# Kernel optimization log

Measured on AMD Instinct MI355X. Metric: run time of the kernel, lower is better.

The kernel has to match this reference:

```python
import jax, jax.numpy as jnp
import numpy as np

B, N = 64, 512
D_ENT, H = 2000, 768
LN_EPS = 1e-12


def setup_inputs() -> dict:
    key = jax.random.key(0)
    ks = jax.random.split(key, 16)
    s = 1.0 / np.sqrt(D_ENT)
    sh = 1.0 / np.sqrt(H)
    return {
        "node_embeddings": jax.random.normal(ks[0], (B, N, D_ENT), jnp.float32),
        "node_types": jax.random.randint(ks[1], (B, N), 0, 2),
        "layers": jax.random.randint(ks[2], (B, N), 0, 8),
        "operators": jax.random.randint(ks[3], (B, N), 0, 2),
        "in_degs": jax.random.randint(ks[4], (B, N), 0, 8),
        "out_degs": jax.random.randint(ks[5], (B, N), 0, 8),
        "negs": jax.random.randint(ks[6], (B, N), 0, 2),
        "type_emb": jax.random.normal(ks[7], (2, H), jnp.float32),
        "layer_emb": jax.random.normal(ks[8], (8, H), jnp.float32),
        "op_emb": jax.random.normal(ks[9], (2, H), jnp.float32),
        "in_emb": jax.random.normal(ks[10], (8, H), jnp.float32),
        "out_emb": jax.random.normal(ks[11], (8, H), jnp.float32),
        "proj_w": jax.random.uniform(ks[12], (H, D_ENT), jnp.float32, -s, s),
        "proj_b": jnp.zeros((H,), jnp.float32),
        "neg_w": jax.random.uniform(ks[13], (H, H), jnp.float32, -sh, sh),
        "neg_b": jnp.zeros((H,), jnp.float32),
        "ln_g": jnp.ones((H,), jnp.float32),
        "ln_b": jnp.zeros((H,), jnp.float32),
    }


def reference(node_embeddings, node_types, layers, operators, in_degs, out_degs, negs,
              type_emb, layer_emb, op_emb, in_emb, out_emb,
              proj_w, proj_b, neg_w, neg_b, ln_g, ln_b):
    # linear projection: [B,N,D_ENT] @ [D_ENT,H]
    x = jnp.einsum("bnd,hd->bnh", node_embeddings, proj_w) + proj_b
    # summed small-table lookups
    x = x + type_emb[node_types] + layer_emb[layers] + op_emb[operators] \
        + in_emb[in_degs] + out_emb[out_degs]
    # rows with negs==1 go through MLP (single Linear h->h); masked select/scatter
    y = jnp.einsum("bnh,gh->bng", x, neg_w) + neg_b
    x = jnp.where((negs == 1)[..., None], y, x)
    # LayerNorm
    mu = jnp.mean(x, axis=-1, keepdims=True)
    var = jnp.mean(jnp.square(x - mu), axis=-1, keepdims=True)
    x = (x - mu) * jax.lax.rsqrt(var + LN_EPS) * ln_g + ln_b
    # dropout is identity in eval mode
    return x
```

## Files before the change

### kernel.cpp

```cpp
#include <hip/hip_runtime.h>
#include <stdint.h>

typedef unsigned short u16;
typedef short v8s __attribute__((ext_vector_type(8)));
typedef float v4f __attribute__((ext_vector_type(4)));

typedef __attribute__((address_space(1))) uint32_t g_u32;
typedef __attribute__((address_space(3))) uint32_t l_u32;

__device__ __forceinline__ void glds16(const void* g, void* l) {
    __builtin_amdgcn_global_load_lds((const g_u32*)g, (l_u32*)l, 16, 0, 0);
}
__device__ __forceinline__ u16 f2b(float f) {
    uint32_t u = __builtin_bit_cast(uint32_t, f);
    u += 0x7FFFu + ((u >> 16) & 1u);
    return (u16)(u >> 16);
}
__device__ __forceinline__ uint32_t pk2(float a, float b) {
    uint32_t ua = __builtin_bit_cast(uint32_t, a) + 0x8000u;
    uint32_t ub = __builtin_bit_cast(uint32_t, b) + 0x8000u;
    return __builtin_amdgcn_perm(ub, ua, 0x07060302u);
}

#define MTOT  32768
#define HDIM  768
#define KDIM  2000
#define KPAD  2016

#define VMW(n) asm volatile("s_waitcnt vmcnt(" #n ")" ::: "memory")
#define BARX do { __builtin_amdgcn_s_barrier(); __builtin_amdgcn_sched_barrier(0); } while (0)

__global__ __launch_bounds__(256) void cvt_weights(
    const float* __restrict__ pw, const float* __restrict__ nw,
    u16* __restrict__ Wb, u16* __restrict__ NWb)
{
    const int h = blockIdx.x;
    const float* src = pw + (size_t)h * KDIM;
    u16* dst = Wb + (size_t)h * KPAD;
    for (int k = threadIdx.x; k < KPAD; k += 256)
        dst[k] = (k < KDIM) ? f2b(src[k]) : (u16)0;
    const float* s2 = nw + (size_t)h * HDIM;
    u16* d2 = NWb + (size_t)h * HDIM;
    for (int k = threadIdx.x; k < HDIM; k += 256)
        d2[k] = f2b(s2[k]);
}

__global__ __launch_bounds__(256) void compact_k(
    const int* __restrict__ negs, int* __restrict__ cmap,
    int* __restrict__ pos, int* __restrict__ cnt)
{
    __shared__ int pref[257];
    const int t = threadIdx.x;
    const int base = t * 128;
    int c = 0;
    for (int j = 0; j < 128; j++) c += (negs[base + j] == 1);
    __shared__ int wsum[256];
    wsum[t] = c;
    __syncthreads();
    if (t == 0) {
        int a = 0;
        for (int i = 0; i < 256; i++) { pref[i] = a; a += wsum[i]; }
        pref[256] = a;
        cnt[0] = a;
    }
    __syncthreads();
    int off = pref[t];
    for (int j = 0; j < 128; j++) {
        const int r = base + j;
        if (negs[r] == 1) { cmap[off] = r; pos[r] = off; off++; }
    }
    const int total = pref[256];
    for (int j = total + t; j < MTOT; j += 256) cmap[j] = 0;
}

__global__ __launch_bounds__(512, 4) void gemm1(
    const float* __restrict__ A, const u16* __restrict__ Wb,
    const float* __restrict__ pb,
    const int* __restrict__ i_ty, const int* __restrict__ i_la,
    const int* __restrict__ i_op, const int* __restrict__ i_in, const int* __restrict__ i_ou,
    const float* __restrict__ te, const float* __restrict__ le, const float* __restrict__ oe,
    const float* __restrict__ ie, const float* __restrict__ ooe,
    u16* __restrict__ Xb)
{
    __shared__ __align__(16) float Asf[2][128 * 32];
    __shared__ __align__(16) u16  Bs[2][256 * 32];

    const int bid = blockIdx.x;
    const int sw = (bid & 7) * 96 + (bid >> 3);
    const int mt = sw / 3, nt = sw % 3;
    const int m_base = mt * 128, n_base = nt * 256;

    const int tid = threadIdx.x;
    const int w = tid >> 6, lane = tid & 63;
    const int lm = lane & 15, quad = lane >> 4;
    const int wm = (w >> 2) * 64, wn = (w & 3) * 64;

    const float* aRowBase[2];
    int aOff[2], aBase[2];
#pragma unroll
    for (int t = 0; t < 2; t++) {
        const int rl = w * 16 + t * 8 + (lane >> 3);
        aRowBase[t] = A + (size_t)(m_base + rl) * KDIM;
        aOff[t] = ((lane & 7) ^ (rl & 7)) * 4;
        aBase[t] = (w * 16 + t * 8) * 32;
    }
    const u16* bSrc[2];
    int bBase[2];
#pragma unroll
    for (int t = 0; t < 2; t++) {
        const int rl = w * 32 + t * 16 + (lane >> 2);
        const int c = (lane & 3) ^ ((rl >> 1) & 3);
        bSrc[t] = Wb + (size_t)(n_base + rl) * KPAD + c * 8;
        bBase[t] = (w * 32 + t * 16) * 32;
    }

    v4f acc[4][4];
#pragma unroll
    for (int i = 0; i < 4; i++)
#pragma unroll
        for (int j = 0; j < 4; j++) acc[i][j] = (v4f){0.f, 0.f, 0.f, 0.f};

    auto issue = [&](int kb) {
        const int sl = kb & 1;
#pragma unroll
        for (int t = 0; t < 2; t++) {
            int k = kb * 32 + aOff[t];
            k = (k > 1996) ? 1996 : k;
            glds16(aRowBase[t] + k, &Asf[sl][aBase[t]]);
        }
#pragma unroll
        for (int t = 0; t < 2; t++)
            glds16(bSrc[t] + kb * 32, &Bs[sl][bBase[t]]);
    };
    auto compute = [&](int kb) {
        const int sl = kb & 1;
        v8s af[4], bf[4];
#pragma unroll
        for (int i = 0; i < 4; i++) {
            const int r = wm + i * 16 + lm;
            const int s8 = r & 7;
            const float4 lo = *(const float4*)&Asf[sl][r * 32 + (((2 * quad)     ^ s8) << 2)];
            const float4 hi = *(const float4*)&Asf[sl][r * 32 + (((2 * quad + 1) ^ s8) << 2)];
            int4 p;
            p.x = (int)pk2(lo.x, lo.y); p.y = (int)pk2(lo.z, lo.w);
            p.z = (int)pk2(hi.x, hi.y); p.w = (int)pk2(hi.z, hi.w);
            af[i] = __builtin_bit_cast(v8s, p);
        }
#pragma unroll
        for (int j = 0; j < 4; j++) {
            const int r = wn + j * 16 + lm;
            bf[j] = *(const v8s*)&Bs[sl][r * 32 + ((quad ^ ((r >> 1) & 3)) << 3)];
        }
#pragma unroll
        for (int i = 0; i < 4; i++)
#pragma unroll
            for (int j = 0; j < 4; j++)
                acc[i][j] = __builtin_amdgcn_mfma_f32_16x16x32_bf16(af[i], bf[j], acc[i][j], 0, 0, 0);
    };

    issue(0);
    issue(1);

    for (int kb = 0; kb < 61; ++kb) {
        VMW(4);
        BARX;
        compute(kb);
        __builtin_amdgcn_sched_barrier(0);
        BARX;
        issue(kb + 2);
    }
    VMW(4); BARX; compute(61);
    __builtin_amdgcn_sched_barrier(0);
    BARX;
    VMW(0); BARX; compute(62);

#pragma unroll
    for (int i = 0; i < 4; i++) {
#pragma unroll
        for (int r = 0; r < 4; r++) {
            const int row = m_base + wm + i * 16 + quad * 4 + r;
            const int ty = i_ty[row], la = i_la[row], op = i_op[row];
            const int di = i_in[row], doo = i_ou[row];
            const float* pte = te + (size_t)ty * HDIM;
            const float* ple = le + (size_t)la * HDIM;
            const float* poe = oe + (size_t)op * HDIM;
            const float* pie = ie + (size_t)di * HDIM;
            const float* pou = ooe + (size_t)doo * HDIM;
            u16* orow = Xb + (size_t)row * HDIM;
#pragma unroll
            for (int j = 0; j < 4; j++) {
                const int col = n_base + wn + j * 16 + lm;
                float v = acc[i][j][r] + pb[col] + pte[col] + ple[col] + poe[col] + pie[col] + pou[col];
                orow[col] = f2b(v);
            }
        }
    }
}

__global__ __launch_bounds__(512, 4) void gemm2(
    const u16* __restrict__ Xb, const u16* __restrict__ NWb,
    const float* __restrict__ nb, const int* __restrict__ cmap,
    const int* __restrict__ cnt, u16* __restrict__ Yb)
{
    __shared__ __align__(16) u16 As[2][128 * 32];
    __shared__ __align__(16) u16 Bs[2][256 * 32];

    const int bid = blockIdx.x;
    const int sw = (bid & 7) * 96 + (bid >> 3);
    const int mt = sw / 3, nt = sw % 3;
    const int m_base = mt * 128, n_base = nt * 256;
    if (m_base >= cnt[0]) return;

    const int tid = threadIdx.x;
    const int w = tid >> 6, lane = tid & 63;
    const int lm = lane & 15, quad = lane >> 4;
    const int wm = (w >> 2) * 64, wn = (w & 3) * 64;

    const int rlA = w * 16 + (lane >> 2);
    const int cAx = (lane & 3) ^ ((rlA >> 1) & 3);
    const u16* aSrc = Xb + (size_t)cmap[m_base + rlA] * HDIM + cAx * 8;
    const int aBase = (w * 16) * 32;
    const u16* bSrc[2];
    int bBase[2];
#pragma unroll
    for (int t = 0; t < 2; t++) {
        const int rl = w * 32 + t * 16 + (lane >> 2);
        const int c = (lane & 3) ^ ((rl >> 1) & 3);
        bSrc[t] = NWb + (size_t)(n_base + rl) * HDIM + c * 8;
        bBase[t] = (w * 32 + t * 16) * 32;
    }

    v4f acc[4][4];
#pragma unroll
    for (int i = 0; i < 4; i++)
#pragma unroll
        for (int j = 0; j < 4; j++) acc[i][j] = (v4f){0.f, 0.f, 0.f, 0.f};

    auto issue = [&](int kb) {
        const int sl = kb & 1;
        glds16(aSrc + kb * 32, &As[sl][aBase]);
#pragma unroll
        for (int t = 0; t < 2; t++)
            glds16(bSrc[t] + kb * 32, &Bs[sl][bBase[t]]);
    };
    auto compute = [&](int kb) {
        const int sl = kb & 1;
        v8s af[4], bf[4];
#pragma unroll
        for (int i = 0; i < 4; i++) {
            const int r = wm + i * 16 + lm;
            af[i] = *(const v8s*)&As[sl][r * 32 + ((quad ^ ((r >> 1) & 3)) << 3)];
        }
#pragma unroll
        for (int j = 0; j < 4; j++) {
            const int r = wn + j * 16 + lm;
            bf[j] = *(const v8s*)&Bs[sl][r * 32 + ((quad ^ ((r >> 1) & 3)) << 3)];
        }
#pragma unroll
        for (int i = 0; i < 4; i++)
#pragma unroll
            for (int j = 0; j < 4; j++)
                acc[i][j] = __builtin_amdgcn_mfma_f32_16x16x32_bf16(af[i], bf[j], acc[i][j], 0, 0, 0);
    };

    issue(0);
    issue(1);

    for (int kb = 0; kb < 22; ++kb) {
        VMW(3);
        BARX;
        compute(kb);
        __builtin_amdgcn_sched_barrier(0);
        BARX;
        issue(kb + 2);
    }
    VMW(3); BARX; compute(22);
    __builtin_amdgcn_sched_barrier(0);
    BARX;
    VMW(0); BARX; compute(23);

#pragma unroll
    for (int i = 0; i < 4; i++) {
#pragma unroll
        for (int r = 0; r < 4; r++) {
            const int crow = m_base + wm + i * 16 + quad * 4 + r;
            u16* orow = Yb + (size_t)crow * HDIM;
#pragma unroll
            for (int j = 0; j < 4; j++) {
                const int col = n_base + wn + j * 16 + lm;
                orow[col] = f2b(acc[i][j][r] + nb[col]);
            }
        }
    }
}

__global__ __launch_bounds__(256) void ln_k(
    const u16* __restrict__ Xb, const u16* __restrict__ Yb,
    const int* __restrict__ negs, const int* __restrict__ pos,
    const float* __restrict__ g, const float* __restrict__ b,
    float* __restrict__ out)
{
    const int w = threadIdx.x >> 6, lane = threadIdx.x & 63;
    const int row = blockIdx.x * 4 + w;
    const u16* src = (negs[row] == 1) ? (Yb + (size_t)pos[row] * HDIM)
                                      : (Xb + (size_t)row * HDIM);

    float v[12];
    float s = 0.f, ss = 0.f;
#pragma unroll
    for (int p = 0; p < 3; p++) {
        uint2 u = *(const uint2*)(src + (p * 64 + lane) * 4);
        float f0 = __builtin_bit_cast(float, u.x << 16);
        float f1 = __builtin_bit_cast(float, u.x & 0xFFFF0000u);
        float f2 = __builtin_bit_cast(float, u.y << 16);
        float f3 = __builtin_bit_cast(float, u.y & 0xFFFF0000u);
        v[p * 4 + 0] = f0; v[p * 4 + 1] = f1; v[p * 4 + 2] = f2; v[p * 4 + 3] = f3;
        s += f0 + f1 + f2 + f3;
        ss += f0 * f0 + f1 * f1 + f2 * f2 + f3 * f3;
    }
#pragma unroll
    for (int off = 1; off < 64; off <<= 1) {
        s += __shfl_xor(s, off);
        ss += __shfl_xor(ss, off);
    }
    const float mean = s * (1.f / (float)HDIM);
    const float var = ss * (1.f / (float)HDIM) - mean * mean;
    const float rs = rsqrtf(var + 1e-12f);

    float* orow = out + (size_t)row * HDIM;
#pragma unroll
    for (int p = 0; p < 3; p++) {
        const int c0 = (p * 64 + lane) * 4;
        float4 gg = *(const float4*)(g + c0);
        float4 bb = *(const float4*)(b + c0);
        float4 o;
        o.x = (v[p * 4 + 0] - mean) * rs * gg.x + bb.x;
        o.y = (v[p * 4 + 1] - mean) * rs * gg.y + bb.y;
        o.z = (v[p * 4 + 2] - mean) * rs * gg.z + bb.z;
        o.w = (v[p * 4 + 3] - mean) * rs * gg.w + bb.w;
        *(float4*)(orow + c0) = o;
    }
}

extern "C" void kernel_launch(void* const* d_in, const int* in_sizes, int n_in,
                              void* d_out, int out_size, void* d_ws, size_t ws_size,
                              hipStream_t stream) {
    (void)in_sizes; (void)n_in; (void)out_size; (void)ws_size;
    const float* A   = (const float*)d_in[0];
    const int* i_ty  = (const int*)d_in[1];
    const int* i_la  = (const int*)d_in[2];
    const int* i_op  = (const int*)d_in[3];
    const int* i_in  = (const int*)d_in[4];
    const int* i_ou  = (const int*)d_in[5];
    const int* negs  = (const int*)d_in[6];
    const float* te  = (const float*)d_in[7];
    const float* le  = (const float*)d_in[8];
    const float* oe  = (const float*)d_in[9];
    const float* ie  = (const float*)d_in[10];
    const float* ooe = (const float*)d_in[11];
    const float* pw  = (const float*)d_in[12];
    const float* pb  = (const float*)d_in[13];
    const float* nw  = (const float*)d_in[14];
    const float* nb  = (const float*)d_in[15];
    const float* lng = (const float*)d_in[16];
    const float* lnb = (const float*)d_in[17];
    float* out = (float*)d_out;

    char* ws = (char*)d_ws;
    u16* Wb  = (u16*)ws;
    u16* NWb = (u16*)(ws + 3096576);
    u16* Xb  = (u16*)(ws + 4276224);
    u16* Yb  = (u16*)(ws + 4276224 + 50331648);
    int* cmap = (int*)(ws + 4276224 + 100663296);
    int* pos  = (int*)(ws + 4276224 + 100663296 + 131072);
    int* cnt  = (int*)(ws + 4276224 + 100663296 + 262144);

    cvt_weights<<<768, 256, 0, stream>>>(pw, nw, Wb, NWb);
    compact_k<<<1, 256, 0, stream>>>(negs, cmap, pos, cnt);
    gemm1<<<768, 512, 0, stream>>>(A, Wb, pb, i_ty, i_la, i_op, i_in, i_ou,
                                   te, le, oe, ie, ooe, Xb);
    gemm2<<<768, 512, 0, stream>>>(Xb, NWb, nb, cmap, cnt, Yb);
    ln_k<<<8192, 256, 0, stream>>>(Xb, Yb, negs, pos, lng, lnb, out);
}
```

Measured before the change: 746.1 us.

## Retile GEMMs to 256x128 with 4 waves and register-staged bf16 A conversion

```diff
diff --git a/kernel.cpp b/kernel.cpp
--- a/kernel.cpp
+++ b/kernel.cpp
@@ -28,6 +28,7 @@
 #define KPAD  2016
 
 #define VMW(n) asm volatile("s_waitcnt vmcnt(" #n ")" ::: "memory")
+#define LGKM0  asm volatile("s_waitcnt lgkmcnt(0)" ::: "memory")
 #define BARX do { __builtin_amdgcn_s_barrier(); __builtin_amdgcn_sched_barrier(0); } while (0)
 
 __global__ __launch_bounds__(256) void cvt_weights(
@@ -50,11 +51,11 @@
     int* __restrict__ pos, int* __restrict__ cnt)
 {
     __shared__ int pref[257];
+    __shared__ int wsum[256];
     const int t = threadIdx.x;
     const int base = t * 128;
     int c = 0;
     for (int j = 0; j < 128; j++) c += (negs[base + j] == 1);
-    __shared__ int wsum[256];
     wsum[t] = c;
     __syncthreads();
     if (t == 0) {
@@ -73,7 +74,7 @@
     for (int j = total + t; j < MTOT; j += 256) cmap[j] = 0;
 }
 
-__global__ __launch_bounds__(512, 4) void gemm1(
+__global__ __launch_bounds__(256) void gemm1(
     const float* __restrict__ A, const u16* __restrict__ Wb,
     const float* __restrict__ pb,
     const int* __restrict__ i_ty, const int* __restrict__ i_la,
@@ -82,69 +83,72 @@
     const float* __restrict__ ie, const float* __restrict__ ooe,
     u16* __restrict__ Xb)
 {
-    __shared__ __align__(16) float Asf[2][128 * 32];
-    __shared__ __align__(16) u16  Bs[2][256 * 32];
+    __shared__ __align__(16) u16 As[2][256 * 32];
+    __shared__ __align__(16) u16 Bs[2][128 * 32];
 
     const int bid = blockIdx.x;
     const int sw = (bid & 7) * 96 + (bid >> 3);
-    const int mt = sw / 3, nt = sw % 3;
-    const int m_base = mt * 128, n_base = nt * 256;
+    const int mt = sw / 6, nt = sw % 6;
+    const int m_base = mt * 256, n_base = nt * 128;
 
     const int tid = threadIdx.x;
     const int w = tid >> 6, lane = tid & 63;
     const int lm = lane & 15, quad = lane >> 4;
-    const int wm = (w >> 2) * 64, wn = (w & 3) * 64;
-
-    const float* aRowBase[2];
-    int aOff[2], aBase[2];
-#pragma unroll
-    for (int t = 0; t < 2; t++) {
-        const int rl = w * 16 + t * 8 + (lane >> 3);
-        aRowBase[t] = A + (size_t)(m_base + rl) * KDIM;
-        aOff[t] = ((lane & 7) ^ (rl & 7)) * 4;
-        aBase[t] = (w * 16 + t * 8) * 32;
+    const int wm = (w >> 1) * 128, wn = (w & 1) * 64;
+
+    const int rsub = lane >> 3, csub = lane & 7;
+    const float* aPtr[8];
+    int aW[8];
+#pragma unroll
+    for (int g = 0; g < 8; g++) {
+        const int rl = w * 64 + g * 8 + rsub;
+        aPtr[g] = A + (size_t)(m_base + rl) * KDIM;
+        aW[g] = rl * 32 + (((csub >> 1) ^ ((rl >> 1) & 3)) << 3) + ((csub & 1) << 2);
     }
     const u16* bSrc[2];
-    int bBase[2];
+    int bDst[2];
 #pragma unroll
     for (int t = 0; t < 2; t++) {
         const int rl = w * 32 + t * 16 + (lane >> 2);
         const int c = (lane & 3) ^ ((rl >> 1) & 3);
         bSrc[t] = Wb + (size_t)(n_base + rl) * KPAD + c * 8;
-        bBase[t] = (w * 32 + t * 16) * 32;
-    }
-
-    v4f acc[4][4];
-#pragma unroll
-    for (int i = 0; i < 4; i++)
+        bDst[t] = (w * 32 + t * 16) * 32;
+    }
+
+    v4f acc[8][4];
+#pragma unroll
+    for (int i = 0; i < 8; i++)
 #pragma unroll
         for (int j = 0; j < 4; j++) acc[i][j] = (v4f){0.f, 0.f, 0.f, 0.f};
 
-    auto issue = [&](int kb) {
+    auto ldA = [&](int kb, float4* r) {
+        int k = kb * 32 + csub * 4;
+        k = (k > 1996) ? 1996 : k;
+#pragma unroll
+        for (int g = 0; g < 8; g++) r[g] = *(const float4*)(aPtr[g] + k);
+    };
+    auto wrA = [&](const float4* r, int sl) {
+#pragma unroll
+        for (int g = 0; g < 8; g++) {
+            uint2 p;
+            p.x = pk2(r[g].x, r[g].y);
+            p.y = pk2(r[g].z, r[g].w);
+            *(uint2*)&As[sl][aW[g]] = p;
+        }
+    };
+    auto stB = [&](int kb) {
         const int sl = kb & 1;
 #pragma unroll
-        for (int t = 0; t < 2; t++) {
-            int k = kb * 32 + aOff[t];
-            k = (k > 1996) ? 1996 : k;
-            glds16(aRowBase[t] + k, &Asf[sl][aBase[t]]);
-        }
-#pragma unroll
         for (int t = 0; t < 2; t++)
-            glds16(bSrc[t] + kb * 32, &Bs[sl][bBase[t]]);
+            glds16(bSrc[t] + kb * 32, &Bs[sl][bDst[t]]);
     };
     auto compute = [&](int kb) {
         const int sl = kb & 1;
-        v8s af[4], bf[4];
-#pragma unroll
-        for (int i = 0; i < 4; i++) {
+        v8s af[8], bf[4];
+#pragma unroll
+        for (int i = 0; i < 8; i++) {
             const int r = wm + i * 16 + lm;
-            const int s8 = r & 7;
-            const float4 lo = *(const float4*)&Asf[sl][r * 32 + (((2 * quad)     ^ s8) << 2)];
-            const float4 hi = *(const float4*)&Asf[sl][r * 32 + (((2 * quad + 1) ^ s8) << 2)];
-            int4 p;
-            p.x = (int)pk2(lo.x, lo.y); p.y = (int)pk2(lo.z, lo.w);
-            p.z = (int)pk2(hi.x, hi.y); p.w = (int)pk2(hi.z, hi.w);
-            af[i] = __builtin_bit_cast(v8s, p);
+            af[i] = *(const v8s*)&As[sl][r * 32 + ((quad ^ ((r >> 1) & 3)) << 3)];
         }
 #pragma unroll
         for (int j = 0; j < 4; j++) {
@@ -152,30 +156,42 @@
             bf[j] = *(const v8s*)&Bs[sl][r * 32 + ((quad ^ ((r >> 1) & 3)) << 3)];
         }
 #pragma unroll
-        for (int i = 0; i < 4; i++)
+        for (int i = 0; i < 8; i++)
 #pragma unroll
             for (int j = 0; j < 4; j++)
                 acc[i][j] = __builtin_amdgcn_mfma_f32_16x16x32_bf16(af[i], bf[j], acc[i][j], 0, 0, 0);
     };
 
-    issue(0);
-    issue(1);
-
-    for (int kb = 0; kb < 61; ++kb) {
-        VMW(4);
+    auto step = [&](int kb, const float4* cur, float4* nxt) {
+        VMW(0);
+        LGKM0;
         BARX;
+        wrA(cur, (kb + 1) & 1);
+        stB(kb + 1);
+        int kn = kb + 2; kn = (kn > 62) ? 62 : kn;
+        ldA(kn, nxt);
         compute(kb);
-        __builtin_amdgcn_sched_barrier(0);
-        BARX;
-        issue(kb + 2);
-    }
-    VMW(4); BARX; compute(61);
-    __builtin_amdgcn_sched_barrier(0);
-    BARX;
-    VMW(0); BARX; compute(62);
-
-#pragma unroll
-    for (int i = 0; i < 4; i++) {
+    };
+
+    float4 aP[8], aN[8];
+    {
+        float4 a0[8];
+        ldA(0, a0);
+        stB(0);
+        ldA(1, aP);
+        VMW(10);
+        wrA(a0, 0);
+    }
+
+    for (int kb = 0; kb < 62; kb += 2) {
+        step(kb,     aP, aN);
+        step(kb + 1, aN, aP);
+    }
+    VMW(0); LGKM0; BARX;
+    compute(62);
+
+#pragma unroll
+    for (int i = 0; i < 8; i++) {
 #pragma unroll
         for (int r = 0; r < 4; r++) {
             const int row = m_base + wm + i * 16 + quad * 4 + r;
@@ -197,57 +213,64 @@
     }
 }
 
-__global__ __launch_bounds__(512, 4) void gemm2(
+__global__ __launch_bounds__(256) void gemm2(
     const u16* __restrict__ Xb, const u16* __restrict__ NWb,
     const float* __restrict__ nb, const int* __restrict__ cmap,
     const int* __restrict__ cnt, u16* __restrict__ Yb)
 {
-    __shared__ __align__(16) u16 As[2][128 * 32];
-    __shared__ __align__(16) u16 Bs[2][256 * 32];
+    __shared__ __align__(16) u16 As[2][256 * 32];
+    __shared__ __align__(16) u16 Bs[2][128 * 32];
 
     const int bid = blockIdx.x;
     const int sw = (bid & 7) * 96 + (bid >> 3);
-    const int mt = sw / 3, nt = sw % 3;
-    const int m_base = mt * 128, n_base = nt * 256;
+    const int mt = sw / 6, nt = sw % 6;
+    const int m_base = mt * 256, n_base = nt * 128;
     if (m_base >= cnt[0]) return;
 
     const int tid = threadIdx.x;
     const int w = tid >> 6, lane = tid & 63;
     const int lm = lane & 15, quad = lane >> 4;
-    const int wm = (w >> 2) * 64, wn = (w & 3) * 64;
-
-    const int rlA = w * 16 + (lane >> 2);
-    const int cAx = (lane & 3) ^ ((rlA >> 1) & 3);
-    const u16* aSrc = Xb + (size_t)cmap[m_base + rlA] * HDIM + cAx * 8;
-    const int aBase = (w * 16) * 32;
+    const int wm = (w >> 1) * 128, wn = (w & 1) * 64;
+
+    const u16* aSrc[4];
+    int aDst[4];
+#pragma unroll
+    for (int t = 0; t < 4; t++) {
+        const int rl = w * 64 + t * 16 + (lane >> 2);
+        const int c = (lane & 3) ^ ((rl >> 1) & 3);
+        aSrc[t] = Xb + (size_t)cmap[m_base + rl] * HDIM + c * 8;
+        aDst[t] = (w * 64 + t * 16) * 32;
+    }
     const u16* bSrc[2];
-    int bBase[2];
+    int bDst[2];
 #pragma unroll
     for (int t = 0; t < 2; t++) {
         const int rl = w * 32 + t * 16 + (lane >> 2);
         const int c = (lane & 3) ^ ((rl >> 1) & 3);
         bSrc[t] = NWb + (size_t)(n_base + rl) * HDIM + c * 8;
-        bBase[t] = (w * 32 + t * 16) * 32;
-    }
-
-    v4f acc[4][4];
-#pragma unroll
-    for (int i = 0; i < 4; i++)
+        bDst[t] = (w * 32 + t * 16) * 32;
+    }
+
+    v4f acc[8][4];
+#pragma unroll
+    for (int i = 0; i < 8; i++)
 #pragma unroll
         for (int j = 0; j < 4; j++) acc[i][j] = (v4f){0.f, 0.f, 0.f, 0.f};
 
-    auto issue = [&](int kb) {
+    auto stage = [&](int kb) {
         const int sl = kb & 1;
-        glds16(aSrc + kb * 32, &As[sl][aBase]);
+#pragma unroll
+        for (int t = 0; t < 4; t++)
+            glds16(aSrc[t] + kb * 32, &As[sl][aDst[t]]);
 #pragma unroll
         for (int t = 0; t < 2; t++)
-            glds16(bSrc[t] + kb * 32, &Bs[sl][bBase[t]]);
+            glds16(bSrc[t] + kb * 32, &Bs[sl][bDst[t]]);
     };
     auto compute = [&](int kb) {
         const int sl = kb & 1;
-        v8s af[4], bf[4];
-#pragma unroll
-        for (int i = 0; i < 4; i++) {
+        v8s af[8], bf[4];
+#pragma unroll
+        for (int i = 0; i < 8; i++) {
             const int r = wm + i * 16 + lm;
             af[i] = *(const v8s*)&As[sl][r * 32 + ((quad ^ ((r >> 1) & 3)) << 3)];
         }
@@ -257,30 +280,24 @@
             bf[j] = *(const v8s*)&Bs[sl][r * 32 + ((quad ^ ((r >> 1) & 3)) << 3)];
         }
 #pragma unroll
-        for (int i = 0; i < 4; i++)
+        for (int i = 0; i < 8; i++)
 #pragma unroll
             for (int j = 0; j < 4; j++)
                 acc[i][j] = __builtin_amdgcn_mfma_f32_16x16x32_bf16(af[i], bf[j], acc[i][j], 0, 0, 0);
     };
 
-    issue(0);
-    issue(1);
-
-    for (int kb = 0; kb < 22; ++kb) {
-        VMW(3);
+    stage(0);
+    for (int kb = 0; kb < 23; ++kb) {
+        VMW(0);
         BARX;
+        stage(kb + 1);
         compute(kb);
-        __builtin_amdgcn_sched_barrier(0);
-        BARX;
-        issue(kb + 2);
-    }
-    VMW(3); BARX; compute(22);
-    __builtin_amdgcn_sched_barrier(0);
-    BARX;
-    VMW(0); BARX; compute(23);
-
-#pragma unroll
-    for (int i = 0; i < 4; i++) {
+    }
+    VMW(0); BARX;
+    compute(23);
+
+#pragma unroll
+    for (int i = 0; i < 8; i++) {
 #pragma unroll
         for (int r = 0; r < 4; r++) {
             const int crow = m_base + wm + i * 16 + quad * 4 + r;
@@ -377,8 +394,8 @@
 
     cvt_weights<<<768, 256, 0, stream>>>(pw, nw, Wb, NWb);
     compact_k<<<1, 256, 0, stream>>>(negs, cmap, pos, cnt);
-    gemm1<<<768, 512, 0, stream>>>(A, Wb, pb, i_ty, i_la, i_op, i_in, i_ou,
+    gemm1<<<768, 256, 0, stream>>>(A, Wb, pb, i_ty, i_la, i_op, i_in, i_ou,
                                    te, le, oe, ie, ooe, Xb);
-    gemm2<<<768, 512, 0, stream>>>(Xb, NWb, nb, cmap, cnt, Yb);
+    gemm2<<<768, 256, 0, stream>>>(Xb, NWb, nb, cmap, cnt, Yb);
     ln_k<<<8192, 256, 0, stream>>>(Xb, Yb, negs, pos, lng, lnb, out);
 }
```

Result: slower. 958.2 us (+28.4%).
